# Optimization experiments

Measured on AMD Instinct MI355X. Metric: run time of the kernel, lower is better.

## Reference

```python
import jax, jax.numpy as jnp
import numpy as np

R = 32768          # rays
S = 128            # fixed step budget per ray (padded/masked)
STEP = 0.02        # step_size
NX = NY = NZ = 256
MINB = jnp.array([-1.0, -1.0, -1.0], jnp.float32)
MAXB = jnp.array([1.0, 1.0, 1.0], jnp.float32)
# voxel sizes: (max - min) / (n - 1)
VOX = (MAXB - MINB) / (jnp.array([NX, NY, NZ], jnp.float32) - 1.0)
N = jnp.array([NX, NY, NZ], jnp.int32)
# 8 corner offsets, same order as the original query_voxels
OFFS = jnp.array([[0,0,0],[1,0,0],[0,1,0],[1,1,0],
                  [0,0,1],[1,0,1],[0,1,1],[1,1,1]], jnp.int32)


def setup_inputs() -> dict:
    key = jax.random.key(0)
    k1, k2, k3 = jax.random.split(key, 3)
    origins = jax.random.uniform(k1, (R, 3), jnp.float32, -0.9, 0.9)
    d = jax.random.normal(k2, (R, 3), jnp.float32)
    directions = d / jnp.linalg.norm(d, axis=-1, keepdims=True)
    sdf_values = jax.random.normal(k3, (NX, NY, NZ), jnp.float32)
    return {"origins": origins, "directions": directions, "sdf_values": sdf_values}


def reference(origins, directions, sdf_values):
    # --- ray_box_intersection (faithful, including the tmin reuse in tmax) ---
    inv_dir = 1.0 / directions                       # [R,3]
    a = (MINB - origins) * inv_dir                   # [R,3]
    b = (MAXB - origins) * inv_dir                   # [R,3]
    t0 = jnp.max(jnp.minimum(a, b), axis=-1)         # [R] scalar tmin
    t1 = jnp.min(jnp.maximum(t0[:, None], b), axis=-1)  # [R] (original overwrites tmin first)
    hit = t1 >= t0                                   # original returns None if tmax < tmin

    # --- march_ray: fixed step grid t = t_near + i*step, masked at t >= t_far ---
    t = t0[:, None] + STEP * jnp.arange(S, dtype=jnp.float32)   # [R,S]
    step_mask = (t < t1[:, None]) & hit[:, None]                # [R,S]
    pts = origins[:, None, :] + t[..., None] * directions[:, None, :]  # [R,S,3]

    # --- query_voxels: truncating index like torch .long() ---
    idx = ((pts - MINB) / VOX).astype(jnp.int32)                # [R,S,3]
    inb = jnp.all((idx >= 0) & (idx < N - 1), axis=-1)          # [R,S]
    valid = inb & step_mask                                     # [R,S]
    idxc = jnp.clip(idx, 0, N - 2)                              # safe gather indices
    ci = idxc[:, :, None, :] + OFFS                             # [R,S,8,3]
    sdf = sdf_values[ci[..., 0], ci[..., 1], ci[..., 2]]        # [R,S,8] 8-corner gather
    sdf = jnp.where(valid[..., None], sdf, 0.0)
    positions = MINB + ci.astype(jnp.float32) * VOX             # [R,S,8,3] corner positions
    positions = jnp.where(valid[..., None, None], positions, 0.0)
    return sdf, positions, valid
```

## Files before the change

kernel.cpp:

```cpp
#include <hip/hip_runtime.h>


constexpr int   RAYS = 32768;
constexpr int   STEPS = 128;
constexpr float STEP = 0.02f;
constexpr float VOX = 2.0f / 255.0f;

typedef float f4 __attribute__((ext_vector_type(4)));
typedef float f2 __attribute__((ext_vector_type(2), aligned(4)));

__global__ __launch_bounds__(256) void sdf_march_kernel(
    const float* __restrict__ org,
    const float* __restrict__ dir,
    const float* __restrict__ sdfv,
    float* __restrict__ out_sdf,
    float* __restrict__ out_pos,
    float* __restrict__ out_valid)
{
#pragma clang fp contract(off)
    __shared__ f4 lds[2048];

    const int tid = threadIdx.x;
    const int gid = blockIdx.x * 256 + tid;
    const int r = gid >> 7;
    const int s = gid & 127;

    const float ox = org[r * 3 + 0], oy = org[r * 3 + 1], oz = org[r * 3 + 2];
    const float dx = dir[r * 3 + 0], dy = dir[r * 3 + 1], dz = dir[r * 3 + 2];

    const float ivx = 1.0f / dx, ivy = 1.0f / dy, ivz = 1.0f / dz;
    const float axv = (-1.0f - ox) * ivx, ayv = (-1.0f - oy) * ivy, azv = (-1.0f - oz) * ivz;
    const float bxv = ( 1.0f - ox) * ivx, byv = ( 1.0f - oy) * ivy, bzv = ( 1.0f - oz) * ivz;
    const float t0 = fmaxf(fmaxf(fminf(axv, bxv), fminf(ayv, byv)), fminf(azv, bzv));
    const float t1 = fminf(fminf(fmaxf(t0, bxv), fmaxf(t0, byv)), fmaxf(t0, bzv));
    const bool hit = (t1 >= t0);

    const float ts = STEP * (float)s;
    const float t  = t0 + ts;
    const bool step_mask = (t < t1) && hit;

    const float mx = t * dx, my = t * dy, mz = t * dz;
    const float px = ox + mx, py = oy + my, pz = oz + mz;

    const float fx = (px + 1.0f) / VOX;
    const float fy = (py + 1.0f) / VOX;
    const float fz = (pz + 1.0f) / VOX;
    const int ix = (int)fx, iy = (int)fy, iz = (int)fz;
    const bool inb = (ix >= 0) & (ix < 255) & (iy >= 0) & (iy < 255) & (iz >= 0) & (iz < 255);
    const bool valid = inb && step_mask;

    const int ixc = min(max(ix, 0), 254);
    const int iyc = min(max(iy, 0), 254);
    const int izc = min(max(iz, 0), 254);

    f4 sv0 = {0.f, 0.f, 0.f, 0.f}, sv1 = {0.f, 0.f, 0.f, 0.f};
    f4 p0 = sv0, p1 = sv0, p2 = sv0, p3 = sv0, p4 = sv0, p5 = sv0;

    if (valid) {
        const int base = (ixc * 256 + iyc) * 256 + izc;
        const f2 vz00 = *(const f2*)(sdfv + base);
        const f2 vz10 = *(const f2*)(sdfv + base + 65536);
        const f2 vz01 = *(const f2*)(sdfv + base + 256);
        const f2 vz11 = *(const f2*)(sdfv + base + 65536 + 256);
        sv0 = (f4){vz00.x, vz10.x, vz01.x, vz11.x};
        sv1 = (f4){vz00.y, vz10.y, vz01.y, vz11.y};

        const float x0 = -1.0f + (float)ixc * VOX;
        const float x1 = -1.0f + (float)(ixc + 1) * VOX;
        const float y0 = -1.0f + (float)iyc * VOX;
        const float y1 = -1.0f + (float)(iyc + 1) * VOX;
        const float z0 = -1.0f + (float)izc * VOX;
        const float z1 = -1.0f + (float)(izc + 1) * VOX;

        p0 = (f4){x0, y0, z0, x1};
        p1 = (f4){y0, z0, x0, y1};
        p2 = (f4){z0, x1, y1, z0};
        p3 = (f4){x0, y0, z1, x1};
        p4 = (f4){y0, z1, x0, y1};
        p5 = (f4){z1, x1, y1, z1};
    }

    f4* lp = lds;
    f4* ls = lds + 1536;
    lp[tid * 6 + 0] = p0;
    lp[tid * 6 + 1] = p1;
    lp[tid * 6 + 2] = p2;
    lp[tid * 6 + 3] = p3;
    lp[tid * 6 + 4] = p4;
    lp[tid * 6 + 5] = p5;
    ls[tid * 2 + 0] = sv0;
    ls[tid * 2 + 1] = sv1;

    __builtin_nontemporal_store(valid ? 1.0f : 0.0f, out_valid + gid);

    __syncthreads();

    f4* op = (f4*)out_pos + (size_t)blockIdx.x * 1536;
#pragma unroll
    for (int k = 0; k < 6; ++k) {
        __builtin_nontemporal_store(lp[tid + 256 * k], op + tid + 256 * k);
    }
    f4* os = (f4*)out_sdf + (size_t)blockIdx.x * 512;
#pragma unroll
    for (int k = 0; k < 2; ++k) {
        __builtin_nontemporal_store(ls[tid + 256 * k], os + tid + 256 * k);
    }
}

extern "C" void kernel_launch(void* const* d_in, const int* in_sizes, int n_in,
                              void* d_out, int out_size, void* d_ws, size_t ws_size,
                              hipStream_t stream) {
    const float* origins    = (const float*)d_in[0];
    const float* directions = (const float*)d_in[1];
    const float* sdf_values = (const float*)d_in[2];

    float* out = (float*)d_out;
    float* out_sdf   = out;
    float* out_pos   = out + 33554432;
    float* out_valid = out + 33554432 + 100663296;

    const int total = RAYS * STEPS;
    dim3 grid(total / 256), block(256);
    sdf_march_kernel<<<grid, block, 0, stream>>>(origins, directions, sdf_values,
                                                 out_sdf, out_pos, out_valid);
}
```

Measured before the change: 594.7 us.

## Halve LDS staging buffer by writing positions in two phases

Shrinks the shared-memory staging area from 32KB to 20KB by staging corner positions for half the block at a time. Two extra barriers separate the phases, and launch bounds now request 8 waves per SIMD. The aim is higher occupancy to hide store and gather latency, at the cost of extra synchronisation and serialised store phases.

```diff
diff --git a/kernel.cpp b/kernel.cpp
--- a/kernel.cpp
+++ b/kernel.cpp
@@ -9,7 +9,7 @@
 typedef float f4 __attribute__((ext_vector_type(4)));
 typedef float f2 __attribute__((ext_vector_type(2), aligned(4)));
 
-__global__ __launch_bounds__(256) void sdf_march_kernel(
+__global__ __launch_bounds__(256, 8) void sdf_march_kernel(
     const float* __restrict__ org,
     const float* __restrict__ dir,
     const float* __restrict__ sdfv,
@@ -18,7 +18,8 @@
     float* __restrict__ out_valid)
 {
 #pragma clang fp contract(off)
-    __shared__ f4 lds[2048];
+    __shared__ f4 lds_pos[768];
+    __shared__ f4 lds_sdf[512];
 
     const int tid = threadIdx.x;
     const int gid = blockIdx.x * 256 + tid;
@@ -54,7 +55,7 @@
     const int izc = min(max(iz, 0), 254);
 
     f4 sv0 = {0.f, 0.f, 0.f, 0.f}, sv1 = {0.f, 0.f, 0.f, 0.f};
-    f4 p0 = sv0, p1 = sv0, p2 = sv0, p3 = sv0, p4 = sv0, p5 = sv0;
+    float x0 = 0.f, x1 = 0.f, y0 = 0.f, y1 = 0.f, z0 = 0.f, z1 = 0.f;
 
     if (valid) {
         const int base = (ixc * 256 + iyc) * 256 + izc;
@@ -65,45 +66,60 @@
         sv0 = (f4){vz00.x, vz10.x, vz01.x, vz11.x};
         sv1 = (f4){vz00.y, vz10.y, vz01.y, vz11.y};
 
-        const float x0 = -1.0f + (float)ixc * VOX;
-        const float x1 = -1.0f + (float)(ixc + 1) * VOX;
-        const float y0 = -1.0f + (float)iyc * VOX;
-        const float y1 = -1.0f + (float)(iyc + 1) * VOX;
-        const float z0 = -1.0f + (float)izc * VOX;
-        const float z1 = -1.0f + (float)(izc + 1) * VOX;
-
-        p0 = (f4){x0, y0, z0, x1};
-        p1 = (f4){y0, z0, x0, y1};
-        p2 = (f4){z0, x1, y1, z0};
-        p3 = (f4){x0, y0, z1, x1};
-        p4 = (f4){y0, z1, x0, y1};
-        p5 = (f4){z1, x1, y1, z1};
+        x0 = -1.0f + (float)ixc * VOX;
+        x1 = -1.0f + (float)(ixc + 1) * VOX;
+        y0 = -1.0f + (float)iyc * VOX;
+        y1 = -1.0f + (float)(iyc + 1) * VOX;
+        z0 = -1.0f + (float)izc * VOX;
+        z1 = -1.0f + (float)(izc + 1) * VOX;
     }
 
-    f4* lp = lds;
-    f4* ls = lds + 1536;
-    lp[tid * 6 + 0] = p0;
-    lp[tid * 6 + 1] = p1;
-    lp[tid * 6 + 2] = p2;
-    lp[tid * 6 + 3] = p3;
-    lp[tid * 6 + 4] = p4;
-    lp[tid * 6 + 5] = p5;
-    ls[tid * 2 + 0] = sv0;
-    ls[tid * 2 + 1] = sv1;
+    const int lrec = tid & 127;
+    const bool lowHalf = (tid < 128);
+
+    lds_sdf[tid * 2 + 0] = sv0;
+    lds_sdf[tid * 2 + 1] = sv1;
+    if (lowHalf) {
+        f4* lp = lds_pos + lrec * 6;
+        lp[0] = (f4){x0, y0, z0, x1};
+        lp[1] = (f4){y0, z0, x0, y1};
+        lp[2] = (f4){z0, x1, y1, z0};
+        lp[3] = (f4){x0, y0, z1, x1};
+        lp[4] = (f4){y0, z1, x0, y1};
+        lp[5] = (f4){z1, x1, y1, z1};
+    }
 
     __builtin_nontemporal_store(valid ? 1.0f : 0.0f, out_valid + gid);
 
     __syncthreads();
 
+    f4* os = (f4*)out_sdf + (size_t)blockIdx.x * 512;
+    __builtin_nontemporal_store(lds_sdf[tid],       os + tid);
+    __builtin_nontemporal_store(lds_sdf[tid + 256], os + tid + 256);
+
     f4* op = (f4*)out_pos + (size_t)blockIdx.x * 1536;
 #pragma unroll
-    for (int k = 0; k < 6; ++k) {
-        __builtin_nontemporal_store(lp[tid + 256 * k], op + tid + 256 * k);
+    for (int k = 0; k < 3; ++k) {
+        __builtin_nontemporal_store(lds_pos[tid + 256 * k], op + tid + 256 * k);
     }
-    f4* os = (f4*)out_sdf + (size_t)blockIdx.x * 512;
+
+    __syncthreads();
+
+    if (!lowHalf) {
+        f4* lp = lds_pos + lrec * 6;
+        lp[0] = (f4){x0, y0, z0, x1};
+        lp[1] = (f4){y0, z0, x0, y1};
+        lp[2] = (f4){z0, x1, y1, z0};
+        lp[3] = (f4){x0, y0, z1, x1};
+        lp[4] = (f4){y0, z1, x0, y1};
+        lp[5] = (f4){z1, x1, y1, z1};
+    }
+
+    __syncthreads();
+
 #pragma unroll
-    for (int k = 0; k < 2; ++k) {
-        __builtin_nontemporal_store(ls[tid + 256 * k], os + tid + 256 * k);
+    for (int k = 0; k < 3; ++k) {
+        __builtin_nontemporal_store(lds_pos[tid + 256 * k], op + 768 + tid + 256 * k);
     }
 }
 
```

Result: no change. 602.5 us (+1.3%).
